# Optimization experiments

Measured on AMD Instinct MI355X. Metric: run time of the kernel, lower is better.

The kernel has to match this reference:

```python
import jax, jax.numpy as jnp
import numpy as np

B, N, C, R = 4, 4096, 64, 16
EPS = 1e-12


def setup_inputs() -> dict:
    key = jax.random.key(0)
    k_x, k_w, k_u = jax.random.split(key, 3)
    x = jax.random.normal(k_x, (B, N, C), dtype=jnp.float32)
    W = jax.random.uniform(k_w, (B, N, N), dtype=jnp.float32)
    # lazily-initialized learnable low-rank factor U ~ 0.01 * randn(N, r)
    U = 0.01 * jax.random.normal(k_u, (N, R), dtype=jnp.float32)
    w_scale = jnp.asarray(1.0, dtype=jnp.float32)
    return {"x": x, "W": W, "U": U, "w_scale": w_scale}


def reference(x, W, U, w_scale):
    # symmetrize adjacency: W <- (W + W^T)/2
    Ws = 0.5 * (W + jnp.swapaxes(W, -1, -2))            # [B,N,N]
    # low-rank symmetric gate A = sigmoid(U U^T), shared over batch
    A = jax.nn.sigmoid(U @ U.T)                          # [N,N]
    K = Ws * A[None, :, :]                               # [B,N,N]
    # degree normalization K <- D^{-1/2} K D^{-1/2}
    # (diag_embed + two bmms in the original == row/col broadcast scaling)
    deg = jnp.maximum(K.sum(axis=-1), EPS)               # [B,N]
    d = jax.lax.rsqrt(deg)                               # [B,N]
    K = K * d[:, :, None] * d[:, None, :]                # [B,N,N]
    # coupling: w_scale * K @ x
    return w_scale * jnp.einsum('bnm,bmc->bnc', K, x)    # [B,N,C]
```

## Files before the change

### kernel.cpp

```cpp
#include <hip/hip_runtime.h>
#include <hip/hip_bf16.h>

#define B_ 4
#define N_ 4096
#define C_ 64
#define R_ 16
#define EPS_ 1e-12f

typedef __attribute__((ext_vector_type(8))) short bf16x8;
typedef __attribute__((ext_vector_type(4))) float f32x4;

static __device__ __forceinline__ unsigned short f2bf(float f) {
    unsigned int u = __float_as_uint(f);
    unsigned int r = (u + 0x7fffu + ((u >> 16) & 1u)) >> 16;
    return (unsigned short)r;
}
static __device__ __forceinline__ float bf2f(unsigned short us) {
    return __uint_as_float(((unsigned int)us) << 16);
}

__global__ __launch_bounds__(256) void k_pass1(
    const float* __restrict__ W, const float* __restrict__ U,
    unsigned short* __restrict__ K0, float* __restrict__ deg)
{
    const int tj = blockIdx.x, ti = blockIdx.y;
    if (ti > tj) return;
    const int I = ti * 64, J = tj * 64;
    const bool diag = (ti == tj);
    const int t = threadIdx.x;
    const int ii = t >> 2, g = t & 3, jjg = g * 16;

    __shared__ float UJ[64][17];
    __shared__ float Wc[64][65];
    __shared__ __align__(16) unsigned short K0s[64][72];
    __shared__ float rsum[64][4];
    __shared__ float csum[64][4];

    {
        const float4 v = *(const float4*)(U + (size_t)(J + (t >> 2)) * R_ + (t & 3) * 4);
        UJ[t >> 2][(t & 3) * 4 + 0] = v.x;
        UJ[t >> 2][(t & 3) * 4 + 1] = v.y;
        UJ[t >> 2][(t & 3) * 4 + 2] = v.z;
        UJ[t >> 2][(t & 3) * 4 + 3] = v.w;
    }
    float ui[16];
    {
        const float* up = U + (size_t)(I + ii) * R_;
        #pragma unroll
        for (int h = 0; h < 4; h++) {
            float4 v = *(const float4*)(up + 4 * h);
            ui[4*h] = v.x; ui[4*h+1] = v.y; ui[4*h+2] = v.z; ui[4*h+3] = v.w;
        }
    }
    __syncthreads();

    float a[16];
    #pragma unroll
    for (int q = 0; q < 16; q++) {
        float s = 0.f;
        #pragma unroll
        for (int k = 0; k < 16; k++) s += ui[k] * UJ[jjg + q][k];
        a[q] = 1.0f / (1.0f + __expf(-s));
    }

    for (int b = 0; b < B_; b++) {
        #pragma unroll
        for (int k = 0; k < 4; k++) {
            int idx = t + 256 * k;
            int row = idx >> 4, c4 = idx & 15;
            const float4 v = *(const float4*)(W + ((size_t)(b * N_ + J + row)) * N_ + I + c4 * 4);
            Wc[row][c4*4+0] = v.x; Wc[row][c4*4+1] = v.y;
            Wc[row][c4*4+2] = v.z; Wc[row][c4*4+3] = v.w;
        }
        float wr[16];
        {
            const float* wp = W + ((size_t)(b * N_ + I + ii)) * N_ + J + jjg;
            #pragma unroll
            for (int h = 0; h < 4; h++) {
                float4 v = *(const float4*)(wp + 4 * h);
                wr[4*h] = v.x; wr[4*h+1] = v.y; wr[4*h+2] = v.z; wr[4*h+3] = v.w;
            }
        }
        __syncthreads();

        float sumI = 0.f;
        unsigned int pk[8];
        #pragma unroll
        for (int q = 0; q < 16; q++) {
            float k0 = 0.5f * (wr[q] + Wc[jjg + q][ii]) * a[q];
            sumI += k0;
            unsigned short us = f2bf(k0);
            if (q & 1) pk[q >> 1] |= ((unsigned int)us) << 16;
            else       pk[q >> 1] = us;
        }
        *(int4*)(&K0s[ii][jjg])     = make_int4(pk[0], pk[1], pk[2], pk[3]);
        *(int4*)(&K0s[ii][jjg + 8]) = make_int4(pk[4], pk[5], pk[6], pk[7]);
        {
            unsigned short* dst = K0 + ((size_t)(b * N_ + I + ii)) * N_ + J + jjg;
            *(int4*)(dst)     = make_int4(pk[0], pk[1], pk[2], pk[3]);
            *(int4*)(dst + 8) = make_int4(pk[4], pk[5], pk[6], pk[7]);
        }
        rsum[ii][g] = sumI;
        __syncthreads();

        if (t < 64) {
            float s = rsum[t][0] + rsum[t][1] + rsum[t][2] + rsum[t][3];
            atomicAdd(deg + b * N_ + I + t, s);
        }
        if (!diag) {
            const int jj = t >> 2, iig = (t & 3) * 16;
            float cs = 0.f;
            unsigned int pko[8];
            #pragma unroll
            for (int q = 0; q < 16; q++) {
                unsigned short us = K0s[iig + q][jj];
                cs += bf2f(us);
                if (q & 1) pko[q >> 1] |= ((unsigned int)us) << 16;
                else       pko[q >> 1] = us;
            }
            unsigned short* dst = K0 + ((size_t)(b * N_ + J + jj)) * N_ + I + iig;
            *(int4*)(dst)     = make_int4(pko[0], pko[1], pko[2], pko[3]);
            *(int4*)(dst + 8) = make_int4(pko[4], pko[5], pko[6], pko[7]);
            csum[jj][t & 3] = cs;
        }
        __syncthreads();

        if (!diag && t < 64) {
            float s = csum[t][0] + csum[t][1] + csum[t][2] + csum[t][3];
            atomicAdd(deg + b * N_ + J + t, s);
        }
    }
}

__global__ __launch_bounds__(256) void k_xdT(
    const float* __restrict__ x, const float* __restrict__ deg,
    unsigned short* __restrict__ xdT)
{
    const int jt = blockIdx.x, b = blockIdx.y;
    const int J = jt * 64, t = threadIdx.x;
    __shared__ float xt[64][68];
    #pragma unroll
    for (int k = 0; k < 4; k++) {
        int idx = t + 256 * k;
        int row = idx >> 4, f4 = idx & 15;
        float d = rsqrtf(fmaxf(deg[b * N_ + J + row], EPS_));
        float4 v = *(const float4*)(x + ((size_t)(b * N_ + J + row)) * C_ + f4 * 4);
        xt[row][f4*4+0] = v.x * d; xt[row][f4*4+1] = v.y * d;
        xt[row][f4*4+2] = v.z * d; xt[row][f4*4+3] = v.w * d;
    }
    __syncthreads();
    const int c = t >> 2, jg = (t & 3) * 16;
    unsigned int pk[8];
    #pragma unroll
    for (int q = 0; q < 16; q++) {
        unsigned short us = f2bf(xt[jg + q][c]);
        if (q & 1) pk[q >> 1] |= ((unsigned int)us) << 16;
        else       pk[q >> 1] = us;
    }
    unsigned short* dst = xdT + ((size_t)(b * C_ + c)) * N_ + J + jg;
    *(int4*)(dst)     = make_int4(pk[0], pk[1], pk[2], pk[3]);
    *(int4*)(dst + 8) = make_int4(pk[4], pk[5], pk[6], pk[7]);
}

__global__ __launch_bounds__(256) void k_gemm(
    const unsigned short* __restrict__ K0, const unsigned short* __restrict__ xdT,
    const float* __restrict__ deg, const float* __restrict__ wsc_p,
    float* __restrict__ out)
{
    const int rb = blockIdx.x, b = blockIdx.y;
    const int I = rb * 32;
    const int t = threadIdx.x, l = t & 63, w = t >> 6;
    __shared__ __align__(16) unsigned short As[32 * 64];
    __shared__ __align__(16) unsigned short Bs[64 * 64];
    f32x4 acc0 = {0.f, 0.f, 0.f, 0.f}, acc1 = {0.f, 0.f, 0.f, 0.f};

    const int ak = (t & 7) * 8;
    const size_t abase  = ((size_t)(b * N_ + I + (t >> 3))) * N_ + ak;
    const size_t bbase0 = ((size_t)(b * C_ + (t >> 3))) * N_ + ak;
    const size_t bbase1 = ((size_t)(b * C_ + 32 + (t >> 3))) * N_ + ak;
    const int rw = (w & 1) * 16, cw = (w >> 1) * 32;
    const int fr = l & 15, fq = l >> 4;

    int4 va  = *(const int4*)(K0  + abase);
    int4 vb0 = *(const int4*)(xdT + bbase0);
    int4 vb1 = *(const int4*)(xdT + bbase1);

    for (int kt = 0; kt < 64; kt++) {
        __syncthreads();
        ((int4*)As)[t]       = va;
        ((int4*)Bs)[t]       = vb0;
        ((int4*)Bs)[256 + t] = vb1;
        __syncthreads();
        if (kt < 63) {
            const int kb = (kt + 1) * 64;
            va  = *(const int4*)(K0  + abase + kb);
            vb0 = *(const int4*)(xdT + bbase0 + kb);
            vb1 = *(const int4*)(xdT + bbase1 + kb);
        }
        #pragma unroll
        for (int kk = 0; kk < 2; kk++) {
            bf16x8 af  = *(const bf16x8*)(As + (rw + fr) * 64 + kk * 32 + fq * 8);
            bf16x8 bf0 = *(const bf16x8*)(Bs + (cw + fr) * 64 + kk * 32 + fq * 8);
            bf16x8 bf1 = *(const bf16x8*)(Bs + (cw + 16 + fr) * 64 + kk * 32 + fq * 8);
            acc0 = __builtin_amdgcn_mfma_f32_16x16x32_bf16(af, bf0, acc0, 0, 0, 0);
            acc1 = __builtin_amdgcn_mfma_f32_16x16x32_bf16(af, bf1, acc1, 0, 0, 0);
        }
    }

    const float wsc = wsc_p[0];
    #pragma unroll
    for (int r = 0; r < 4; r++) {
        int row = I + rw + fq * 4 + r;
        float sc = wsc * rsqrtf(fmaxf(deg[b * N_ + row], EPS_));
        out[((size_t)(b * N_ + row)) * C_ + cw + fr]      = sc * acc0[r];
        out[((size_t)(b * N_ + row)) * C_ + cw + 16 + fr] = sc * acc1[r];
    }
}

extern "C" void kernel_launch(void* const* d_in, const int* in_sizes, int n_in,
                              void* d_out, int out_size, void* d_ws, size_t ws_size,
                              hipStream_t stream)
{
    const float* x   = (const float*)d_in[0];
    const float* W   = (const float*)d_in[1];
    const float* U   = (const float*)d_in[2];
    const float* wsc = (const float*)d_in[3];
    float* out = (float*)d_out;

    unsigned short* K0  = (unsigned short*)d_ws;
    float*          deg = (float*)((char*)d_ws + (size_t)B_ * N_ * N_ * 2);
    unsigned short* xdT = (unsigned short*)((char*)deg + (size_t)B_ * N_ * 4);

    hipMemsetAsync(deg, 0, (size_t)B_ * N_ * sizeof(float), stream);
    hipLaunchKernelGGL(k_pass1, dim3(64, 64), dim3(256), 0, stream, W, U, K0, deg);
    hipLaunchKernelGGL(k_xdT,  dim3(64, 4),  dim3(256), 0, stream, x, deg, xdT);
    hipLaunchKernelGGL(k_gemm, dim3(128, 4), dim3(256), 0, stream, K0, xdT, deg, wsc, out);
}
```

Measured before the change: 468.0 us.

## Prefetch next-batch W tiles, shuffle-reduce degrees, and stream GEMM operands directly

The pass1 kernel now loads the next batch's W tiles into registers while the current batch is processed, so the W reads overlap with compute. Row and column degree sums now use wavefront shuffles and atomics instead of shared-memory reductions, which removes a barrier. The transposed write-back is reorganized to read 32-bit pairs from shared memory. The GEMM drops LDS staging and has each wave load its MFMA fragments straight from global memory, using 16-row blocks and twice as many blocks; this trades fewer barriers for less operand reuse and more global or cache traffic.

```diff
diff --git a/kernel.cpp b/kernel.cpp
--- a/kernel.cpp
+++ b/kernel.cpp
@@ -33,8 +33,6 @@
     __shared__ float UJ[64][17];
     __shared__ float Wc[64][65];
     __shared__ __align__(16) unsigned short K0s[64][72];
-    __shared__ float rsum[64][4];
-    __shared__ float csum[64][4];
 
     {
         const float4 v = *(const float4*)(U + (size_t)(J + (t >> 2)) * R_ + (t & 3) * 4);
@@ -43,6 +41,17 @@
         UJ[t >> 2][(t & 3) * 4 + 2] = v.z;
         UJ[t >> 2][(t & 3) * 4 + 3] = v.w;
     }
+
+    float4 wcv[4], wrv[4], wcvN[4], wrvN[4];
+    #pragma unroll
+    for (int k = 0; k < 4; k++) {
+        const int idx = t + 256 * k, row = idx >> 4, c4 = idx & 15;
+        wcv[k] = *(const float4*)(W + ((size_t)(0 * N_ + J + row)) * N_ + I + c4 * 4);
+    }
+    #pragma unroll
+    for (int h = 0; h < 4; h++)
+        wrv[h] = *(const float4*)(W + ((size_t)(0 * N_ + I + ii)) * N_ + J + jjg + 4 * h);
+
     float ui[16];
     {
         const float* up = U + (size_t)(I + ii) * R_;
@@ -63,31 +72,32 @@
         a[q] = 1.0f / (1.0f + __expf(-s));
     }
 
+    #pragma unroll
+    for (int k = 0; k < 4; k++) {
+        const int idx = t + 256 * k, row = idx >> 4, c4 = idx & 15;
+        Wc[row][c4*4+0] = wcv[k].x; Wc[row][c4*4+1] = wcv[k].y;
+        Wc[row][c4*4+2] = wcv[k].z; Wc[row][c4*4+3] = wcv[k].w;
+    }
+    __syncthreads();
+
     for (int b = 0; b < B_; b++) {
-        #pragma unroll
-        for (int k = 0; k < 4; k++) {
-            int idx = t + 256 * k;
-            int row = idx >> 4, c4 = idx & 15;
-            const float4 v = *(const float4*)(W + ((size_t)(b * N_ + J + row)) * N_ + I + c4 * 4);
-            Wc[row][c4*4+0] = v.x; Wc[row][c4*4+1] = v.y;
-            Wc[row][c4*4+2] = v.z; Wc[row][c4*4+3] = v.w;
-        }
-        float wr[16];
-        {
-            const float* wp = W + ((size_t)(b * N_ + I + ii)) * N_ + J + jjg;
-            #pragma unroll
-            for (int h = 0; h < 4; h++) {
-                float4 v = *(const float4*)(wp + 4 * h);
-                wr[4*h] = v.x; wr[4*h+1] = v.y; wr[4*h+2] = v.z; wr[4*h+3] = v.w;
-            }
-        }
-        __syncthreads();
-
+        if (b < B_ - 1) {
+            #pragma unroll
+            for (int k = 0; k < 4; k++) {
+                const int idx = t + 256 * k, row = idx >> 4, c4 = idx & 15;
+                wcvN[k] = *(const float4*)(W + ((size_t)((b+1) * N_ + J + row)) * N_ + I + c4 * 4);
+            }
+            #pragma unroll
+            for (int h = 0; h < 4; h++)
+                wrvN[h] = *(const float4*)(W + ((size_t)((b+1) * N_ + I + ii)) * N_ + J + jjg + 4 * h);
+        }
+
+        const float* wrf = (const float*)wrv;
         float sumI = 0.f;
         unsigned int pk[8];
         #pragma unroll
         for (int q = 0; q < 16; q++) {
-            float k0 = 0.5f * (wr[q] + Wc[jjg + q][ii]) * a[q];
+            float k0 = 0.5f * (wrf[q] + Wc[jjg + q][ii]) * a[q];
             sumI += k0;
             unsigned short us = f2bf(k0);
             if (q & 1) pk[q >> 1] |= ((unsigned int)us) << 16;
@@ -100,34 +110,50 @@
             *(int4*)(dst)     = make_int4(pk[0], pk[1], pk[2], pk[3]);
             *(int4*)(dst + 8) = make_int4(pk[4], pk[5], pk[6], pk[7]);
         }
-        rsum[ii][g] = sumI;
+        {
+            float s = sumI + __shfl_xor(sumI, 1, 64);
+            s += __shfl_xor(s, 2, 64);
+            if (g == 0) atomicAdd(deg + b * N_ + I + ii, s);
+        }
         __syncthreads();
 
-        if (t < 64) {
-            float s = rsum[t][0] + rsum[t][1] + rsum[t][2] + rsum[t][3];
-            atomicAdd(deg + b * N_ + I + t, s);
-        }
         if (!diag) {
-            const int jj = t >> 2, iig = (t & 3) * 16;
-            float cs = 0.f;
-            unsigned int pko[8];
-            #pragma unroll
-            for (int q = 0; q < 16; q++) {
-                unsigned short us = K0s[iig + q][jj];
-                cs += bf2f(us);
-                if (q & 1) pko[q >> 1] |= ((unsigned int)us) << 16;
-                else       pko[q >> 1] = us;
-            }
-            unsigned short* dst = K0 + ((size_t)(b * N_ + J + jj)) * N_ + I + iig;
-            *(int4*)(dst)     = make_int4(pko[0], pko[1], pko[2], pko[3]);
-            *(int4*)(dst + 8) = make_int4(pko[4], pko[5], pko[6], pko[7]);
-            csum[jj][t & 3] = cs;
-        }
-        __syncthreads();
-
-        if (!diag && t < 64) {
-            float s = csum[t][0] + csum[t][1] + csum[t][2] + csum[t][3];
-            atomicAdd(deg + b * N_ + J + t, s);
+            const int c2 = t & 31, r8 = t >> 5;
+            unsigned int v[8];
+            float cs0 = 0.f, cs1 = 0.f;
+            #pragma unroll
+            for (int k = 0; k < 8; k++) {
+                v[k] = *(const unsigned int*)(&K0s[r8 * 8 + k][c2 * 2]);
+                cs0 += bf2f((unsigned short)(v[k] & 0xffffu));
+                cs1 += bf2f((unsigned short)(v[k] >> 16));
+            }
+            unsigned int plo[4], phi[4];
+            #pragma unroll
+            for (int m = 0; m < 4; m++) {
+                plo[m] = (v[2*m] & 0xffffu) | (v[2*m+1] << 16);
+                phi[m] = (v[2*m] >> 16) | (v[2*m+1] & 0xffff0000u);
+            }
+            unsigned short* dst0 = K0 + ((size_t)(b * N_ + J + 2 * c2)) * N_ + I + r8 * 8;
+            unsigned short* dst1 = dst0 + N_;
+            *(int4*)dst0 = make_int4(plo[0], plo[1], plo[2], plo[3]);
+            *(int4*)dst1 = make_int4(phi[0], phi[1], phi[2], phi[3]);
+            cs0 += __shfl_xor(cs0, 32, 64);
+            cs1 += __shfl_xor(cs1, 32, 64);
+            if ((t & 32) == 0) {
+                atomicAdd(deg + b * N_ + J + 2 * c2,     cs0);
+                atomicAdd(deg + b * N_ + J + 2 * c2 + 1, cs1);
+            }
+        }
+        if (b < B_ - 1) {
+            #pragma unroll
+            for (int k = 0; k < 4; k++) {
+                const int idx = t + 256 * k, row = idx >> 4, c4 = idx & 15;
+                Wc[row][c4*4+0] = wcvN[k].x; Wc[row][c4*4+1] = wcvN[k].y;
+                Wc[row][c4*4+2] = wcvN[k].z; Wc[row][c4*4+3] = wcvN[k].w;
+            }
+            #pragma unroll
+            for (int h = 0; h < 4; h++) wrv[h] = wrvN[h];
+            __syncthreads();
         }
     }
 }
@@ -138,7 +164,7 @@
 {
     const int jt = blockIdx.x, b = blockIdx.y;
     const int J = jt * 64, t = threadIdx.x;
-    __shared__ float xt[64][68];
+    __shared__ float xt[64][69];
     #pragma unroll
     for (int k = 0; k < 4; k++) {
         int idx = t + 256 * k;
@@ -168,52 +194,31 @@
     float* __restrict__ out)
 {
     const int rb = blockIdx.x, b = blockIdx.y;
-    const int I = rb * 32;
+    const int I = rb * 16;
     const int t = threadIdx.x, l = t & 63, w = t >> 6;
-    __shared__ __align__(16) unsigned short As[32 * 64];
-    __shared__ __align__(16) unsigned short Bs[64 * 64];
+    const int fr = l & 15, fq = l >> 4, cw = w * 16;
+
+    const unsigned short* Ap = K0  + ((size_t)(b * N_ + I + fr)) * N_ + fq * 8;
+    const unsigned short* Bp = xdT + ((size_t)(b * C_ + cw + fr)) * N_ + fq * 8;
+
     f32x4 acc0 = {0.f, 0.f, 0.f, 0.f}, acc1 = {0.f, 0.f, 0.f, 0.f};
-
-    const int ak = (t & 7) * 8;
-    const size_t abase  = ((size_t)(b * N_ + I + (t >> 3))) * N_ + ak;
-    const size_t bbase0 = ((size_t)(b * C_ + (t >> 3))) * N_ + ak;
-    const size_t bbase1 = ((size_t)(b * C_ + 32 + (t >> 3))) * N_ + ak;
-    const int rw = (w & 1) * 16, cw = (w >> 1) * 32;
-    const int fr = l & 15, fq = l >> 4;
-
-    int4 va  = *(const int4*)(K0  + abase);
-    int4 vb0 = *(const int4*)(xdT + bbase0);
-    int4 vb1 = *(const int4*)(xdT + bbase1);
-
-    for (int kt = 0; kt < 64; kt++) {
-        __syncthreads();
-        ((int4*)As)[t]       = va;
-        ((int4*)Bs)[t]       = vb0;
-        ((int4*)Bs)[256 + t] = vb1;
-        __syncthreads();
-        if (kt < 63) {
-            const int kb = (kt + 1) * 64;
-            va  = *(const int4*)(K0  + abase + kb);
-            vb0 = *(const int4*)(xdT + bbase0 + kb);
-            vb1 = *(const int4*)(xdT + bbase1 + kb);
-        }
-        #pragma unroll
-        for (int kk = 0; kk < 2; kk++) {
-            bf16x8 af  = *(const bf16x8*)(As + (rw + fr) * 64 + kk * 32 + fq * 8);
-            bf16x8 bf0 = *(const bf16x8*)(Bs + (cw + fr) * 64 + kk * 32 + fq * 8);
-            bf16x8 bf1 = *(const bf16x8*)(Bs + (cw + 16 + fr) * 64 + kk * 32 + fq * 8);
-            acc0 = __builtin_amdgcn_mfma_f32_16x16x32_bf16(af, bf0, acc0, 0, 0, 0);
-            acc1 = __builtin_amdgcn_mfma_f32_16x16x32_bf16(af, bf1, acc1, 0, 0, 0);
-        }
-    }
+    #pragma unroll 8
+    for (int k = 0; k < N_; k += 64) {
+        bf16x8 a0 = *(const bf16x8*)(Ap + k);
+        bf16x8 b0 = *(const bf16x8*)(Bp + k);
+        bf16x8 a1 = *(const bf16x8*)(Ap + k + 32);
+        bf16x8 b1 = *(const bf16x8*)(Bp + k + 32);
+        acc0 = __builtin_amdgcn_mfma_f32_16x16x32_bf16(a0, b0, acc0, 0, 0, 0);
+        acc1 = __builtin_amdgcn_mfma_f32_16x16x32_bf16(a1, b1, acc1, 0, 0, 0);
+    }
+    f32x4 acc = acc0 + acc1;
 
     const float wsc = wsc_p[0];
     #pragma unroll
     for (int r = 0; r < 4; r++) {
-        int row = I + rw + fq * 4 + r;
-        float sc = wsc * rsqrtf(fmaxf(deg[b * N_ + row], EPS_));
-        out[((size_t)(b * N_ + row)) * C_ + cw + fr]      = sc * acc0[r];
-        out[((size_t)(b * N_ + row)) * C_ + cw + 16 + fr] = sc * acc1[r];
+        const int row = I + fq * 4 + r;
+        const float sc = wsc * rsqrtf(fmaxf(deg[b * N_ + row], EPS_));
+        out[((size_t)(b * N_ + row)) * C_ + cw + fr] = sc * acc[r];
     }
 }
 
@@ -233,6 +238,6 @@
 
     hipMemsetAsync(deg, 0, (size_t)B_ * N_ * sizeof(float), stream);
     hipLaunchKernelGGL(k_pass1, dim3(64, 64), dim3(256), 0, stream, W, U, K0, deg);
-    hipLaunchKernelGGL(k_xdT,  dim3(64, 4),  dim3(256), 0, stream, x, deg, xdT);
-    hipLaunchKernelGGL(k_gemm, dim3(128, 4), dim3(256), 0, stream, K0, xdT, deg, wsc, out);
-}
+    hipLaunchKernelGGL(k_xdT,  dim3(64, 4),   dim3(256), 0, stream, x, deg, xdT);
+    hipLaunchKernelGGL(k_gemm, dim3(256, 4),  dim3(256), 0, stream, K0, xdT, deg, wsc, out);
+}
```

New measurement: 522.1 us. +11.6%, slower.
